# Performance work log

Hardware: AMD Instinct MI355X
Metric: run time of the kernel (lower is better)

## Reference

```python
import jax, jax.numpy as jnp
import numpy as np

NW, K, C, H = 4096, 32, 256, 8
HD = C // H
POS_BND = 25            # int(0.8 * patch_size * dilation**0.5) = int(0.8*32)
RPE_NUM = 2 * POS_BND + 1  # 51; table has 3*51 = 153 rows


def setup_inputs() -> dict:
    key = jax.random.key(0)
    ks = jax.random.split(key, 10)
    s = 0.02
    return {
        "data": jax.random.normal(ks[0], (NW * K, C), jnp.float32),
        "mask": jax.random.normal(ks[1], (NW, K, K), jnp.float32),
        "rel_pos": jax.random.randint(ks[2], (NW, K, K, 3), -POS_BND, POS_BND + 1, jnp.int32),
        "qkv_w": jax.random.normal(ks[3], (C, 3 * C), jnp.float32) * s,
        "qkv_b": jnp.zeros((3 * C,), jnp.float32),
        "proj_w": jax.random.normal(ks[4], (C, C), jnp.float32) * s,
        "proj_b": jnp.zeros((C,), jnp.float32),
        "rpe_table": jax.random.normal(ks[5], (3 * RPE_NUM, H), jnp.float32) * s,
        "ln1_g": jnp.ones((C,), jnp.float32),
        "ln1_b": jnp.zeros((C,), jnp.float32),
        "ln2_g": jnp.ones((C,), jnp.float32),
        "ln2_b": jnp.zeros((C,), jnp.float32),
        "fc1_w": jax.random.normal(ks[6], (C, 4 * C), jnp.float32) * s,
        "fc1_b": jnp.zeros((4 * C,), jnp.float32),
        "fc2_w": jax.random.normal(ks[7], (4 * C, C), jnp.float32) * s,
        "fc2_b": jnp.zeros((C,), jnp.float32),
    }


def _ln(x, g, b):
    m = jnp.mean(x, axis=-1, keepdims=True)
    v = jnp.var(x, axis=-1, keepdims=True)
    return (x - m) * jax.lax.rsqrt(v + 1e-5) * g + b


def reference(data, mask, rel_pos, qkv_w, qkv_b, proj_w, proj_b, rpe_table,
              ln1_g, ln1_b, ln2_g, ln2_b, fc1_w, fc1_b, fc2_w, fc2_b):
    scale = float(HD) ** -0.5
    # pre-norm attention branch
    x = _ln(data, ln1_g, ln1_b)
    qkv = (x @ qkv_w + qkv_b).reshape(NW, K, 3, H, HD)
    q, k, v = qkv[:, :, 0], qkv[:, :, 1], qkv[:, :, 2]   # [NW,K,H,HD]
    attn = jnp.einsum('wqhd,wkhd->whqk', q * scale, k)   # [NW,H,K,K]
    # RPE: clamp xyz offsets, offset each axis into its table band, gather+sum
    idx = jnp.clip(rel_pos, -POS_BND, POS_BND) + POS_BND + jnp.arange(3) * RPE_NUM
    bias = rpe_table[idx].sum(axis=3)                    # [NW,K,K,H]
    attn = attn + bias.transpose(0, 3, 1, 2) + mask[:, None]
    attn = jax.nn.softmax(attn, axis=-1)
    out = jnp.einsum('whqk,wkhd->wqhd', attn, v).reshape(NW * K, C)
    data = data + (out @ proj_w + proj_b)
    # pre-norm MLP branch
    h = _ln(data, ln2_g, ln2_b)
    h = jax.nn.gelu(h @ fc1_w + fc1_b) @ fc2_w + fc2_b
    return data + h
```

## Files before the change

kernel.cpp:

```cpp
#include <hip/hip_runtime.h>

#define NWIN 4096
#define KTOK 32
#define CH 256
#define NH 8
#define NTOK (NWIN*KTOK)

typedef unsigned short bf16u;
typedef __attribute__((ext_vector_type(4))) float f32x4;
typedef __attribute__((ext_vector_type(4))) unsigned short u16x4;
typedef __attribute__((ext_vector_type(8))) unsigned short u16x8;
typedef __attribute__((ext_vector_type(8))) __bf16 bf16x8;

__device__ __forceinline__ unsigned short f2bf(float f) {
  unsigned u = __builtin_bit_cast(unsigned, f);
  u += 0x7fffu + ((u >> 16) & 1u);
  return (unsigned short)(u >> 16);
}

__device__ __forceinline__ f32x4 mfma16(bf16x8 a, bf16x8 b, f32x4 c) {
  return __builtin_amdgcn_mfma_f32_16x16x32_bf16(a, b, c, 0, 0, 0);
}

__device__ __forceinline__ float gelu_f(float x) {
  float u = x + 0.044715f * x * x * x;
  return x / (1.f + __expf(-1.5957691216057308f * u));
}

__global__ __launch_bounds__(256) void wprep_kernel(const float* __restrict__ W,
                                                    bf16u* __restrict__ Wt,
                                                    int Kd, int Nd) {
  int idx = blockIdx.x * 256 + threadIdx.x;
  if (idx >= Kd * Nd) return;
  int k = idx / Nd, n = idx - k * Nd;
  Wt[n * Kd + k] = f2bf(W[idx]);
}

__global__ __launch_bounds__(256) void ln_kernel(const float* __restrict__ x,
                                                 const float* __restrict__ g,
                                                 const float* __restrict__ b,
                                                 bf16u* __restrict__ y) {
  const int row = blockIdx.x * 4 + (threadIdx.x >> 6);
  const int lane = threadIdx.x & 63;
  const size_t base = (size_t)row * CH + lane * 4;
  const f32x4 v = *(const f32x4*)(x + base);
  float s = v[0] + v[1] + v[2] + v[3];
  float q = v[0]*v[0] + v[1]*v[1] + v[2]*v[2] + v[3]*v[3];
  #pragma unroll
  for (int d = 32; d; d >>= 1) { s += __shfl_xor(s, d); q += __shfl_xor(q, d); }
  const float mean = s * (1.f/256.f);
  const float rs = rsqrtf(q * (1.f/256.f) - mean*mean + 1e-5f);
  const f32x4 gv = *(const f32x4*)(g + lane*4);
  const f32x4 bv = *(const f32x4*)(b + lane*4);
  u16x4 o;
  #pragma unroll
  for (int d = 0; d < 4; ++d) o[d] = f2bf((v[d]-mean)*rs*gv[d] + bv[d]);
  *(u16x4*)(y + base) = o;
}

template<int EPI>
__global__ __launch_bounds__(256, 2)
void gemm_kernel(const bf16u* __restrict__ A, const bf16u* __restrict__ Bt,
                 const float* __restrict__ bias, const float* __restrict__ resid,
                 void* __restrict__ out, int M, int N, int K) {
  __shared__ __align__(16) char lds[16384];
  const int tid = threadIdx.x;
  const int lane = tid & 63;
  const int wv = tid >> 6;
  const int lo = lane & 15, hi = lane >> 4;
  const int bm = blockIdx.y * 128, bn = blockIdx.x * 128;
  const int wm = (wv >> 1) * 64, wn = (wv & 1) * 64;
  char* As = lds;
  char* Bs = lds + 8192;

  f32x4 acc[4][4] = {};

  for (int k0 = 0; k0 < K; k0 += 32) {
    __syncthreads();
    #pragma unroll
    for (int t = 0; t < 2; ++t) {
      const int c = tid + t*256;
      const int row = c >> 2;
      const int ck = (c & 3) * 8;
      u16x8 va = *(const u16x8*)(A + (size_t)(bm + row) * K + k0 + ck);
      u16x8 vb = *(const u16x8*)(Bt + (size_t)(bn + row) * K + k0 + ck);
      *(u16x8*)(As + row*64 + ck*2) = va;
      *(u16x8*)(Bs + row*64 + ck*2) = vb;
    }
    __syncthreads();
    bf16x8 af[4], bfv[4];
    #pragma unroll
    for (int i = 0; i < 4; ++i) {
      af[i]  = *(const bf16x8*)(As + (wm + i*16 + lo)*64 + hi*16);
      bfv[i] = *(const bf16x8*)(Bs + (wn + i*16 + lo)*64 + hi*16);
    }
    #pragma unroll
    for (int i = 0; i < 4; ++i)
      #pragma unroll
      for (int j = 0; j < 4; ++j)
        acc[i][j] = mfma16(af[i], bfv[j], acc[i][j]);
  }

  const int mb = bm + wm, nb = bn + wn;
  #pragma unroll
  for (int i = 0; i < 4; ++i) {
    #pragma unroll
    for (int j = 0; j < 4; ++j) {
      const int n = nb + j*16 + lo;
      const float bv = bias[n];
      #pragma unroll
      for (int r = 0; r < 4; ++r) {
        const int m = mb + i*16 + hi*4 + r;
        float v = acc[i][j][r] + bv;
        if constexpr (EPI == 2) {
          v += resid[(size_t)m*N + n];
          ((float*)out)[(size_t)m*N + n] = v;
        } else {
          if constexpr (EPI == 1) v = gelu_f(v);
          ((bf16u*)out)[(size_t)m*N + n] = f2bf(v);
        }
      }
    }
  }
}

__global__ __launch_bounds__(256, 2)
void attn_kernel(const bf16u* __restrict__ qkv, const float* __restrict__ mask,
                 const int* __restrict__ relp, const float* __restrict__ rpe,
                 bf16u* __restrict__ outp) {
  const int w = blockIdx.x;
  const int tid = threadIdx.x, lane = tid & 63, wv = tid >> 6;
  const int lo = lane & 15, hi = lane >> 4;

  __shared__ __align__(16) bf16u sQK[32*520];
  __shared__ __align__(16) bf16u sVT[8][32][40];
  __shared__ __align__(16) bf16u sP[4][32][40];
  __shared__ float sTab[1232];
  __shared__ int sRel[1024];
  __shared__ float sMask[1024];

  const size_t qbase = (size_t)w * (32*768);
  {
    #pragma unroll
    for (int t = 0; t < 8; ++t) {
      int i = tid + t*256;
      int tok = i >> 6;
      int cb = (i & 63) * 16;
      *(u16x8*)((char*)sQK + tok*1040 + cb) =
          *(const u16x8*)((const char*)(qkv + qbase) + tok*1536 + cb);
    }
    #pragma unroll
    for (int t = 0; t < 4; ++t) {
      int i = tid + t*256;
      int tok = i >> 5, c8 = i & 31;
      int h = c8 >> 2, d0 = (c8 & 3) * 8;
      u16x8 v8 = *(const u16x8*)(qkv + qbase + tok*768 + 512 + c8*8);
      #pragma unroll
      for (int j = 0; j < 8; ++j) sVT[h][d0 + j][tok] = v8[j];
    }
    for (int i = tid; i < 1224; i += 256) sTab[i] = rpe[i];
    #pragma unroll
    for (int t = 0; t < 4; ++t) {
      int i = tid + t*256;
      const int* rp = relp + ((size_t)w*1024 + i)*3;
      int r0 = rp[0], r1 = rp[1], r2 = rp[2];
      r0 = min(max(r0, -25), 25) + 25;
      r1 = min(max(r1, -25), 25) + 76;
      r2 = min(max(r2, -25), 25) + 127;
      sRel[i] = r0 | (r1 << 8) | (r2 << 16);
    }
    *(f32x4*)(sMask + tid*4) = *(const f32x4*)(mask + (size_t)w*1024 + tid*4);
  }
  __syncthreads();

  const float scale = 0.17677669529663687f;
  #pragma unroll
  for (int e = 0; e < 2; ++e) {
    const int h = wv*2 + e;
    bf16x8 qf[2], kf[2];
    #pragma unroll
    for (int rf = 0; rf < 2; ++rf) {
      int tok = rf*16 + lo;
      qf[rf] = *(const bf16x8*)((const char*)sQK + tok*1040 + h*64 + hi*16);
      kf[rf] = *(const bf16x8*)((const char*)sQK + tok*1040 + 512 + h*64 + hi*16);
    }
    f32x4 S[2][2] = {};
    #pragma unroll
    for (int rf = 0; rf < 2; ++rf)
      #pragma unroll
      for (int cf = 0; cf < 2; ++cf)
        S[rf][cf] = mfma16(qf[rf], kf[cf], S[rf][cf]);
    #pragma unroll
    for (int rf = 0; rf < 2; ++rf)
      #pragma unroll
      for (int cf = 0; cf < 2; ++cf)
        #pragma unroll
        for (int r = 0; r < 4; ++r) {
          const int qq = rf*16 + hi*4 + r;
          const int kk = cf*16 + lo;
          const int pk = sRel[qq*32 + kk];
          const float bsum = sTab[(pk & 255)*8 + h] + sTab[((pk >> 8) & 255)*8 + h]
                           + sTab[((pk >> 16) & 255)*8 + h];
          S[rf][cf][r] = S[rf][cf][r] * scale + bsum + sMask[qq*32 + kk];
        }
    #pragma unroll
    for (int rf = 0; rf < 2; ++rf)
      #pragma unroll
      for (int r = 0; r < 4; ++r) {
        float m0 = fmaxf(S[rf][0][r], S[rf][1][r]);
        #pragma unroll
        for (int d = 1; d < 16; d <<= 1) m0 = fmaxf(m0, __shfl_xor(m0, d));
        const float p0 = __expf(S[rf][0][r] - m0);
        const float p1 = __expf(S[rf][1][r] - m0);
        float ss = p0 + p1;
        #pragma unroll
        for (int d = 1; d < 16; d <<= 1) ss += __shfl_xor(ss, d);
        const float inv = 1.f / ss;
        S[rf][0][r] = p0 * inv;
        S[rf][1][r] = p1 * inv;
      }
    #pragma unroll
    for (int rf = 0; rf < 2; ++rf)
      #pragma unroll
      for (int cf = 0; cf < 2; ++cf)
        #pragma unroll
        for (int r = 0; r < 4; ++r)
          sP[wv][rf*16 + hi*4 + r][cf*16 + lo] = f2bf(S[rf][cf][r]);
    bf16x8 pf[2], vf[2];
    #pragma unroll
    for (int rf = 0; rf < 2; ++rf) {
      pf[rf] = *(const bf16x8*)&sP[wv][rf*16 + lo][hi*8];
      vf[rf] = *(const bf16x8*)&sVT[h][rf*16 + lo][hi*8];
    }
    f32x4 O[2][2] = {};
    #pragma unroll
    for (int rf = 0; rf < 2; ++rf)
      #pragma unroll
      for (int cf = 0; cf < 2; ++cf)
        O[rf][cf] = mfma16(pf[rf], vf[cf], O[rf][cf]);
    #pragma unroll
    for (int rf = 0; rf < 2; ++rf)
      #pragma unroll
      for (int cf = 0; cf < 2; ++cf)
        #pragma unroll
        for (int r = 0; r < 4; ++r) {
          const int qq = rf*16 + hi*4 + r;
          outp[(size_t)(w*32 + qq)*256 + h*32 + cf*16 + lo] = f2bf(O[rf][cf][r]);
        }
  }
}

extern "C" void kernel_launch(void* const* d_in, const int* in_sizes, int n_in,
                              void* d_out, int out_size, void* d_ws, size_t ws_size,
                              hipStream_t stream) {
  const float* data   = (const float*)d_in[0];
  const float* mask   = (const float*)d_in[1];
  const int*   relp   = (const int*)d_in[2];
  const float* qkv_w  = (const float*)d_in[3];
  const float* qkv_b  = (const float*)d_in[4];
  const float* proj_w = (const float*)d_in[5];
  const float* proj_b = (const float*)d_in[6];
  const float* rpe    = (const float*)d_in[7];
  const float* ln1_g  = (const float*)d_in[8];
  const float* ln1_b  = (const float*)d_in[9];
  const float* ln2_g  = (const float*)d_in[10];
  const float* ln2_b  = (const float*)d_in[11];
  const float* fc1_w  = (const float*)d_in[12];
  const float* fc1_b  = (const float*)d_in[13];
  const float* fc2_w  = (const float*)d_in[14];
  const float* fc2_b  = (const float*)d_in[15];

  char* ws = (char*)d_ws;
  bf16u* wt_qkv  = (bf16u*)(ws);
  bf16u* wt_proj = (bf16u*)(ws + 393216);
  bf16u* wt_fc1  = (bf16u*)(ws + 524288);
  bf16u* wt_fc2  = (bf16u*)(ws + 1048576);
  bf16u* xbuf    = (bf16u*)(ws + 2097152);
  bf16u* qkvbuf  = (bf16u*)(ws + 2097152 + 67108864);
  float* data2   = (float*)d_out;

  wprep_kernel<<<768, 256, 0, stream>>>(qkv_w, wt_qkv, 256, 768);
  wprep_kernel<<<256, 256, 0, stream>>>(proj_w, wt_proj, 256, 256);
  wprep_kernel<<<1024, 256, 0, stream>>>(fc1_w, wt_fc1, 256, 1024);
  wprep_kernel<<<1024, 256, 0, stream>>>(fc2_w, wt_fc2, 1024, 256);

  ln_kernel<<<32768, 256, 0, stream>>>(data, ln1_g, ln1_b, xbuf);
  gemm_kernel<0><<<dim3(6, 1024), 256, 0, stream>>>(xbuf, wt_qkv, qkv_b, nullptr,
                                                    qkvbuf, NTOK, 768, 256);
  attn_kernel<<<NWIN, 256, 0, stream>>>(qkvbuf, mask, relp, rpe, xbuf);
  gemm_kernel<2><<<dim3(2, 1024), 256, 0, stream>>>(xbuf, wt_proj, proj_b, data,
                                                    data2, NTOK, 256, 256);
  ln_kernel<<<32768, 256, 0, stream>>>(data2, ln2_g, ln2_b, xbuf);
  gemm_kernel<1><<<dim3(8, 1024), 256, 0, stream>>>(xbuf, wt_fc1, fc1_b, nullptr,
                                                    qkvbuf, NTOK, 1024, 256);
  gemm_kernel<2><<<dim3(2, 1024), 256, 0, stream>>>(qkvbuf, wt_fc2, fc2_b, data2,
                                                    d_out, NTOK, 256, 1024);
}
```

Before: 752.2 us.

## Use direct global-to-LDS loads, XCD-aware block swizzle, and bank-friendlier attention LDS layouts

```diff
diff --git a/kernel.cpp b/kernel.cpp
--- a/kernel.cpp
+++ b/kernel.cpp
@@ -20,6 +20,12 @@
 
 __device__ __forceinline__ f32x4 mfma16(bf16x8 a, bf16x8 b, f32x4 c) {
   return __builtin_amdgcn_mfma_f32_16x16x32_bf16(a, b, c, 0, 0, 0);
+}
+
+__device__ __forceinline__ void gl16(const void* g, void* l) {
+  __builtin_amdgcn_global_load_lds(
+      (const __attribute__((address_space(1))) unsigned int*)g,
+      (__attribute__((address_space(3))) unsigned int*)l, 16, 0, 0);
 }
 
 __device__ __forceinline__ float gelu_f(float x) {
@@ -62,31 +68,37 @@
 __global__ __launch_bounds__(256, 2)
 void gemm_kernel(const bf16u* __restrict__ A, const bf16u* __restrict__ Bt,
                  const float* __restrict__ bias, const float* __restrict__ resid,
-                 void* __restrict__ out, int M, int N, int K) {
+                 void* __restrict__ out, int M, int N, int K, int nx) {
   __shared__ __align__(16) char lds[16384];
   const int tid = threadIdx.x;
   const int lane = tid & 63;
   const int wv = tid >> 6;
   const int lo = lane & 15, hi = lane >> 4;
-  const int bm = blockIdx.y * 128, bn = blockIdx.x * 128;
+  const int nwg = gridDim.x;
+  const int cpx = nwg >> 3;
+  const int swz = (blockIdx.x & 7) * cpx + (blockIdx.x >> 3);
+  const int by = swz / nx, bx = swz - by * nx;
+  const int bm = by * 128, bn = bx * 128;
   const int wm = (wv >> 1) * 64, wn = (wv & 1) * 64;
   char* As = lds;
   char* Bs = lds + 8192;
 
   f32x4 acc[4][4] = {};
 
+  const int srow = tid >> 2;
+  const int sk = (tid & 3) * 16;
+  const size_t rstep = (size_t)64 * K * 2;
+  const char* gA = (const char*)(A + (size_t)(bm + srow) * K) + sk;
+  const char* gB = (const char*)(Bt + (size_t)(bn + srow) * K) + sk;
+
   for (int k0 = 0; k0 < K; k0 += 32) {
     __syncthreads();
-    #pragma unroll
-    for (int t = 0; t < 2; ++t) {
-      const int c = tid + t*256;
-      const int row = c >> 2;
-      const int ck = (c & 3) * 8;
-      u16x8 va = *(const u16x8*)(A + (size_t)(bm + row) * K + k0 + ck);
-      u16x8 vb = *(const u16x8*)(Bt + (size_t)(bn + row) * K + k0 + ck);
-      *(u16x8*)(As + row*64 + ck*2) = va;
-      *(u16x8*)(Bs + row*64 + ck*2) = vb;
-    }
+    const char* ga = gA + k0 * 2;
+    const char* gb = gB + k0 * 2;
+    gl16(ga,         As + tid*16);
+    gl16(ga + rstep, As + 4096 + tid*16);
+    gl16(gb,         Bs + tid*16);
+    gl16(gb + rstep, Bs + 4096 + tid*16);
     __syncthreads();
     bf16x8 af[4], bfv[4];
     #pragma unroll
@@ -133,11 +145,11 @@
   const int lo = lane & 15, hi = lane >> 4;
 
   __shared__ __align__(16) bf16u sQK[32*520];
-  __shared__ __align__(16) bf16u sVT[8][32][40];
-  __shared__ __align__(16) bf16u sP[4][32][40];
-  __shared__ float sTab[1232];
+  __shared__ __align__(16) bf16u sV[32][264];
+  __shared__ __align__(16) bf16u sP[4][32][44];
+  __shared__ float sTabT[8][156];
   __shared__ int sRel[1024];
-  __shared__ float sMask[1024];
+  __shared__ float sMask[32][33];
 
   const size_t qbase = (size_t)w * (32*768);
   {
@@ -153,12 +165,10 @@
     for (int t = 0; t < 4; ++t) {
       int i = tid + t*256;
       int tok = i >> 5, c8 = i & 31;
-      int h = c8 >> 2, d0 = (c8 & 3) * 8;
-      u16x8 v8 = *(const u16x8*)(qkv + qbase + tok*768 + 512 + c8*8);
-      #pragma unroll
-      for (int j = 0; j < 8; ++j) sVT[h][d0 + j][tok] = v8[j];
-    }
-    for (int i = tid; i < 1224; i += 256) sTab[i] = rpe[i];
+      *(u16x8*)&sV[tok][c8*8] = *(const u16x8*)(qkv + qbase + tok*768 + 512 + c8*8);
+    }
+    for (int i = tid; i < 1224; i += 256)
+      sTabT[i & 7][i >> 3] = rpe[i];
     #pragma unroll
     for (int t = 0; t < 4; ++t) {
       int i = tid + t*256;
@@ -169,7 +179,11 @@
       r2 = min(max(r2, -25), 25) + 127;
       sRel[i] = r0 | (r1 << 8) | (r2 << 16);
     }
-    *(f32x4*)(sMask + tid*4) = *(const f32x4*)(mask + (size_t)w*1024 + tid*4);
+    #pragma unroll
+    for (int d = 0; d < 4; ++d) {
+      int i = tid*4 + d;
+      sMask[i >> 5][i & 31] = mask[(size_t)w*1024 + i];
+    }
   }
   __syncthreads();
 
@@ -199,9 +213,9 @@
           const int qq = rf*16 + hi*4 + r;
           const int kk = cf*16 + lo;
           const int pk = sRel[qq*32 + kk];
-          const float bsum = sTab[(pk & 255)*8 + h] + sTab[((pk >> 8) & 255)*8 + h]
-                           + sTab[((pk >> 16) & 255)*8 + h];
-          S[rf][cf][r] = S[rf][cf][r] * scale + bsum + sMask[qq*32 + kk];
+          const float bsum = sTabT[h][pk & 255] + sTabT[h][(pk >> 8) & 255]
+                           + sTabT[h][(pk >> 16) & 255];
+          S[rf][cf][r] = S[rf][cf][r] * scale + bsum + sMask[qq][kk];
         }
     #pragma unroll
     for (int rf = 0; rf < 2; ++rf)
@@ -226,18 +240,21 @@
         #pragma unroll
         for (int r = 0; r < 4; ++r)
           sP[wv][rf*16 + hi*4 + r][cf*16 + lo] = f2bf(S[rf][cf][r]);
-    bf16x8 pf[2], vf[2];
+    f32x4 O[2][2] = {};
     #pragma unroll
     for (int rf = 0; rf < 2; ++rf) {
-      pf[rf] = *(const bf16x8*)&sP[wv][rf*16 + lo][hi*8];
-      vf[rf] = *(const bf16x8*)&sVT[h][rf*16 + lo][hi*8];
-    }
-    f32x4 O[2][2] = {};
-    #pragma unroll
-    for (int rf = 0; rf < 2; ++rf)
-      #pragma unroll
-      for (int cf = 0; cf < 2; ++cf)
-        O[rf][cf] = mfma16(pf[rf], vf[cf], O[rf][cf]);
+      bf16x8 pf;
+      *(u16x4*)&pf       = *(const u16x4*)&sP[wv][rf*16 + lo][hi*8];
+      *((u16x4*)&pf + 1) = *(const u16x4*)&sP[wv][rf*16 + lo][hi*8 + 4];
+      #pragma unroll
+      for (int cf = 0; cf < 2; ++cf) {
+        bf16x8 vf;
+        #pragma unroll
+        for (int j = 0; j < 8; ++j)
+          ((bf16u*)&vf)[j] = sV[hi*8 + j][h*32 + cf*16 + lo];
+        O[rf][cf] = mfma16(pf, vf, O[rf][cf]);
+      }
+    }
     #pragma unroll
     for (int rf = 0; rf < 2; ++rf)
       #pragma unroll
@@ -285,14 +302,14 @@
   wprep_kernel<<<1024, 256, 0, stream>>>(fc2_w, wt_fc2, 1024, 256);
 
   ln_kernel<<<32768, 256, 0, stream>>>(data, ln1_g, ln1_b, xbuf);
-  gemm_kernel<0><<<dim3(6, 1024), 256, 0, stream>>>(xbuf, wt_qkv, qkv_b, nullptr,
-                                                    qkvbuf, NTOK, 768, 256);
+  gemm_kernel<0><<<6*1024, 256, 0, stream>>>(xbuf, wt_qkv, qkv_b, nullptr,
+                                             qkvbuf, NTOK, 768, 256, 6);
   attn_kernel<<<NWIN, 256, 0, stream>>>(qkvbuf, mask, relp, rpe, xbuf);
-  gemm_kernel<2><<<dim3(2, 1024), 256, 0, stream>>>(xbuf, wt_proj, proj_b, data,
-                                                    data2, NTOK, 256, 256);
+  gemm_kernel<2><<<2*1024, 256, 0, stream>>>(xbuf, wt_proj, proj_b, data,
+                                             data2, NTOK, 256, 256, 2);
   ln_kernel<<<32768, 256, 0, stream>>>(data2, ln2_g, ln2_b, xbuf);
-  gemm_kernel<1><<<dim3(8, 1024), 256, 0, stream>>>(xbuf, wt_fc1, fc1_b, nullptr,
-                                                    qkvbuf, NTOK, 1024, 256);
-  gemm_kernel<2><<<dim3(2, 1024), 256, 0, stream>>>(qkvbuf, wt_fc2, fc2_b, data2,
-                                                    d_out, NTOK, 256, 1024);
-}
+  gemm_kernel<1><<<8*1024, 256, 0, stream>>>(xbuf, wt_fc1, fc1_b, nullptr,
+                                             qkvbuf, NTOK, 1024, 256, 8);
+  gemm_kernel<2><<<2*1024, 256, 0, stream>>>(qkvbuf, wt_fc2, fc2_b, data2,
+                                             d_out, NTOK, 256, 1024, 2);
+}
```

Measured after the change: 668.4 us. -11.1%, faster.
